# Kernel optimization log

Hardware: AMD Instinct MI355X
Metric: run time of the kernel (lower is better)

Reference implementation:

```python
import jax, jax.numpy as jnp
import numpy as np


def setup_inputs() -> dict:
    key = jax.random.key(0)
    ks = jax.random.split(key, 10)
    B, C, H, W = 2, 256, 48, 48
    Ch = 32  # C_qk // n_heads
    s = 1.0 / np.sqrt(C)
    return {
        "x": jax.random.normal(ks[0], (B, C, H, W), jnp.float32),
        "y": jax.random.normal(ks[1], (B, C, H, W), jnp.float32),
        "wq": jax.random.normal(ks[2], (C, C), jnp.float32) * s,
        "bq": jnp.zeros((C,), jnp.float32),
        "wk": jax.random.normal(ks[3], (C, C), jnp.float32) * s,
        "bk": jnp.zeros((C,), jnp.float32),
        "wv": jax.random.normal(ks[4], (C, C), jnp.float32) * s,
        "bv": jnp.zeros((C,), jnp.float32),
        "wo": jax.random.normal(ks[5], (C, C), jnp.float32) * s,
        "bo": jnp.zeros((C,), jnp.float32),
        "h_emb": jax.random.normal(ks[6], (2 * H - 1, Ch), jnp.float32),
        "w_emb": jax.random.normal(ks[7], (2 * W - 1, Ch), jnp.float32),
        "n_heads": 8,
    }


def _rel_grids(H, W):
    yi, xi = np.meshgrid(np.arange(H), np.arange(W), indexing="ij")
    rel_y = yi.reshape(1, -1) - yi.reshape(-1, 1) + (H - 1)  # [HW, HW]
    rel_x = xi.reshape(1, -1) - xi.reshape(-1, 1) + (W - 1)
    return jnp.asarray(rel_y), jnp.asarray(rel_x)


def reference(x, y, wq, bq, wk, bk, wv, bv, wo, bo, h_emb, w_emb, n_heads):
    B, C, H, W = x.shape
    HW = H * W
    C_qk = wq.shape[0]
    flat_x = x.reshape(B, C, HW)
    flat_y = y.reshape(B, C, HW)
    # 1x1 conv1d projections == matmul over channel dim
    q = jnp.einsum("oc,bcn->bon", wq, flat_x) + bq[None, :, None]
    k = jnp.einsum("oc,bcn->bon", wk, flat_y) + bk[None, :, None]
    v = jnp.einsum("oc,bcn->bon", wv, flat_y) + bv[None, :, None]
    Ch = C_qk // n_heads
    q = q.reshape(B, n_heads, Ch, HW)
    k = k.reshape(B, n_heads, Ch, HW)
    v = v.reshape(B, n_heads, Ch, HW)
    score = jnp.einsum("bhcq,bhck->bhqk", q, k)
    # relative positional bias: Q . (R_x + R_y)
    rel_y, rel_x = _rel_grids(H, W)
    r = w_emb[rel_x] + h_emb[rel_y]  # [HW, HW, Ch]
    score = score + jnp.einsum("bhci,ijc->bhij", q, r)
    score = score * (1.0 / jnp.sqrt(jnp.float32(C_qk)))
    attn = jax.nn.softmax(score, axis=-1)
    attn_out = jnp.einsum("bhqk,bhck->bhcq", attn, v).reshape(B, C, H, W)
    out = jnp.einsum("oc,bchw->bohw", wo, attn_out) + bo[None, :, None, None]
    return out
```

## Files before the change

### kernel.cpp

```cpp
#include <hip/hip_runtime.h>
#include <hip/hip_bf16.h>
#include <math.h>

#define HWN 2304
#define CC  256
#define NHD 8
#define CHD 32

#define QT_OFF 0
#define KT_OFF (2 * HWN * CC)
#define OP_OFF (2 * KT_OFF)
#define KBH_OFF (OP_OFF + 16 * HWN * CHD)
#define KBL_OFF (KBH_OFF + (16 * HWN * CHD) / 2)
#define VB_OFF  (KBL_OFF + (16 * HWN * CHD) / 2)
#define BD_OFF  (VB_OFF + 16 * HWN * CHD)

typedef __attribute__((ext_vector_type(8))) short bf16x8;
typedef __attribute__((ext_vector_type(4))) short bf16x4;
typedef __attribute__((ext_vector_type(4))) float f32x4;

__device__ inline unsigned short bf16_rne(float f) {
    unsigned int u = __float_as_uint(f);
    unsigned int r = u + 0x7FFFu + ((u >> 16) & 1u);
    return (unsigned short)(r >> 16);
}
__device__ inline float bf16_to_f(unsigned short h) {
    return __uint_as_float(((unsigned int)h) << 16);
}
__device__ inline bf16x4 bc4(int a, int b) {
    int2 t = make_int2(a, b);
    return __builtin_bit_cast(bf16x4, t);
}

__device__ inline f32x4 mfma32(bf16x8 a, bf16x8 b, f32x4 c) {
    return __builtin_amdgcn_mfma_f32_16x16x32_bf16(a, b, c, 0, 0, 0);
}
__device__ inline f32x4 mfma16(bf16x4 a, bf16x4 b, f32x4 c) {
#if __has_builtin(__builtin_amdgcn_mfma_f32_16x16x16bf16_1k)
    return __builtin_amdgcn_mfma_f32_16x16x16bf16_1k(a, b, c, 0, 0, 0);
#else
    f32x4 d;
    asm volatile("v_mfma_f32_16x16x16_bf16 %0, %1, %2, %3"
                 : "=v"(d) : "v"(a), "v"(b), "v"(c));
    return d;
#endif
}

__global__ __launch_bounds__(256) void proj_kernel(
    const float* __restrict__ x, const float* __restrict__ y,
    const float* __restrict__ wq, const float* __restrict__ bq,
    const float* __restrict__ wk, const float* __restrict__ bk,
    const float* __restrict__ wv, const float* __restrict__ bv,
    float* __restrict__ ws)
{
    const int nb = blockIdx.x * 64;
    const int ob = blockIdx.y * 64;
    const int z  = blockIdx.z;
    const int b = z / 3, which = z % 3;
    const float* in  = (which == 0) ? x : y;
    const float* W   = (which == 0) ? wq : (which == 1) ? wk : wv;
    const float* bia = (which == 0) ? bq : (which == 1) ? bk : bv;

    __shared__ float Xs[64][68];
    __shared__ float Wn[64][68];

    const int t  = threadIdx.x;
    const int tn = t & 15, to = t >> 4;
    float acc[4][4] = {};

    for (int cc = 0; cc < CC; cc += 64) {
        const int r   = t >> 4;
        const int col = (t & 15) * 4;
        #pragma unroll
        for (int rr = 0; rr < 4; rr++) {
            const int row = r + rr * 16;
            *(float4*)&Xs[row][col] =
                *(const float4*)&in[((size_t)b * CC + cc + row) * HWN + nb + col];
            *(float4*)&Wn[row][col] =
                *(const float4*)&W[(size_t)(ob + row) * CC + cc + col];
        }
        __syncthreads();
        #pragma unroll 4
        for (int k = 0; k < 64; k++) {
            float av[4];
            #pragma unroll
            for (int i2 = 0; i2 < 4; i2++) av[i2] = Wn[to * 4 + i2][k];
            const float4 b4 = *(const float4*)&Xs[k][tn * 4];
            const float bv4[4] = {b4.x, b4.y, b4.z, b4.w};
            #pragma unroll
            for (int i2 = 0; i2 < 4; i2++)
                #pragma unroll
                for (int j2 = 0; j2 < 4; j2++)
                    acc[i2][j2] = fmaf(av[i2], bv4[j2], acc[i2][j2]);
        }
        __syncthreads();
    }
    float bb[4];
    *(float4*)bb = *(const float4*)&bia[ob + to * 4];

    if (which < 2) {
        float* out = ws + ((which == 0) ? QT_OFF : KT_OFF) + (size_t)b * HWN * CC;
        #pragma unroll
        for (int j2 = 0; j2 < 4; j2++) {
            const int n = nb + tn * 4 + j2;
            float4 vo = { acc[0][j2] + bb[0], acc[1][j2] + bb[1],
                          acc[2][j2] + bb[2], acc[3][j2] + bb[3] };
            *(float4*)&out[(size_t)n * CC + ob + to * 4] = vo;
        }
    }
    if (which == 1) {
        const int o0  = ob + to * 4;
        const int b8h = b * NHD + (o0 >> 5);
        const int c0i = o0 & 31;
        unsigned short* bh_hi = (unsigned short*)(ws + KBH_OFF);
        unsigned short* bh_lo = (unsigned short*)(ws + KBL_OFF);
        #pragma unroll
        for (int j2 = 0; j2 < 4; j2++) {
            const int n = nb + tn * 4 + j2;
            unsigned int hh[2] = {0, 0}, ll[2] = {0, 0};
            #pragma unroll
            for (int i2 = 0; i2 < 4; i2++) {
                float v = acc[i2][j2] + bb[i2];
                unsigned short h = bf16_rne(v);
                unsigned short l = bf16_rne(v - bf16_to_f(h));
                hh[i2 >> 1] |= ((unsigned int)h) << ((i2 & 1) * 16);
                ll[i2 >> 1] |= ((unsigned int)l) << ((i2 & 1) * 16);
            }
            const size_t idx = ((size_t)b8h * HWN + n) * CHD + c0i;
            *(uint2*)(bh_hi + idx) = make_uint2(hh[0], hh[1]);
            *(uint2*)(bh_lo + idx) = make_uint2(ll[0], ll[1]);
        }
    } else if (which == 2) {
        const int o0  = ob + to * 4;
        const int b8h = b * NHD + (o0 >> 5);
        const int c0i = o0 & 31;
        unsigned short* vb = (unsigned short*)(ws + VB_OFF);
        #pragma unroll
        for (int i2 = 0; i2 < 4; i2++) {
            unsigned int hh[2] = {0, 0}, ll[2] = {0, 0};
            #pragma unroll
            for (int j2 = 0; j2 < 4; j2++) {
                float v = acc[i2][j2] + bb[i2];
                unsigned short h = bf16_rne(v);
                unsigned short l = bf16_rne(v - bf16_to_f(h));
                hh[j2 >> 1] |= ((unsigned int)h) << ((j2 & 1) * 16);
                ll[j2 >> 1] |= ((unsigned int)l) << ((j2 & 1) * 16);
            }
            const size_t off = (((size_t)b8h * CHD + c0i + i2) * 576
                                + (nb >> 2) + tn) * 8;
            uint4 pk = { hh[0], hh[1], ll[0], ll[1] };
            *(uint4*)(vb + off) = pk;
        }
    }
}

__global__ __launch_bounds__(256) void bounds_kernel(
    const float* __restrict__ h_emb, const float* __restrict__ w_emb,
    float* __restrict__ ws)
{
    const float* Kt = ws + KT_OFF;
    float* bounds = ws + BD_OFF;
    __shared__ float red[256];
    const int t = threadIdx.x;
    const int bh = blockIdx.x;
    if (bh < 16) {
        const int b = bh >> 3, h = bh & 7;
        float mx = 0.f;
        for (int j = t; j < HWN; j += 256) {
            const float* kp = &Kt[((size_t)b * HWN + j) * CC + h * CHD];
            float s = 0.f;
            #pragma unroll
            for (int c = 0; c < CHD; c += 4) {
                float4 v = *(const float4*)&kp[c];
                s += v.x * v.x + v.y * v.y + v.z * v.z + v.w * v.w;
            }
            mx = fmaxf(mx, s);
        }
        red[t] = mx; __syncthreads();
        for (int s2 = 128; s2 > 0; s2 >>= 1) {
            if (t < s2) red[t] = fmaxf(red[t], red[t + s2]);
            __syncthreads();
        }
        if (t == 0) bounds[bh] = sqrtf(red[0]);
    } else {
        float mw = 0.f, mh = 0.f;
        if (t < 95) {
            float s = 0.f;
            for (int c = 0; c < CHD; c++) { float v = w_emb[t * CHD + c]; s += v * v; }
            mw = s;
            s = 0.f;
            for (int c = 0; c < CHD; c++) { float v = h_emb[t * CHD + c]; s += v * v; }
            mh = s;
        }
        red[t] = mw; __syncthreads();
        for (int s2 = 128; s2 > 0; s2 >>= 1) {
            if (t < s2) red[t] = fmaxf(red[t], red[t + s2]);
            __syncthreads();
        }
        const float rw = red[0]; __syncthreads();
        red[t] = mh; __syncthreads();
        for (int s2 = 128; s2 > 0; s2 >>= 1) {
            if (t < s2) red[t] = fmaxf(red[t], red[t + s2]);
            __syncthreads();
        }
        if (t == 0) bounds[16] = sqrtf(rw) + sqrtf(red[0]);
    }
}

__global__ __launch_bounds__(256, 3) void attn_kernel(
    const float* __restrict__ h_emb, const float* __restrict__ w_emb,
    float* __restrict__ ws)
{
    const float* Qt = ws + QT_OFF;
    const float* bounds = ws + BD_OFF;
    const unsigned short* Kbh = (const unsigned short*)(ws + KBH_OFF);
    const unsigned short* Kbl = (const unsigned short*)(ws + KBL_OFF);
    const unsigned short* Vb  = (const unsigned short*)(ws + VB_OFF);
    float* OP = ws + OP_OFF;

    __shared__ float lds_a[5376];
    __shared__ float lds_b[4704];

    const int t = threadIdx.x;
    const int wv = t >> 6;
    const int lane = t & 63;
    const int il = lane & 15;
    const int g  = lane >> 4;

    const int gid = blockIdx.y * 48 + blockIdx.x;
    const int xcd = gid & 7;
    const int idx = gid >> 3;
    const int sub = idx / 48;
    const int yi  = idx - sub * 48;
    const int bh  = xcd * 2 + sub;
    const int b = bh >> 3, h = bh & 7;
    const float c1 = 0.09016844005556021f;

    bf16x8 qhi[3], qlo[3];
    float c0[3];
    {
        const float bsum = bounds[bh] + bounds[16];
        #pragma unroll
        for (int isub = 0; isub < 3; isub++) {
            const float* qp = Qt + ((size_t)(b * HWN + yi * 48 + isub * 16 + il)) * CC
                              + h * CHD + g * 8;
            float qf[8];
            *(float4*)&qf[0] = *(const float4*)qp;
            *(float4*)&qf[4] = *(const float4*)(qp + 4);
            float qn = 0.f;
            #pragma unroll
            for (int e = 0; e < 8; e++) qn = fmaf(qf[e], qf[e], qn);
            qn += __shfl_xor(qn, 16);
            qn += __shfl_xor(qn, 32);
            c0[isub] = -sqrtf(qn) * bsum * c1;
            #pragma unroll
            for (int e = 0; e < 8; e++) {
                unsigned short hh = bf16_rne(qf[e]);
                qhi[isub][e] = (short)hh;
                qlo[isub][e] = (short)bf16_rne(qf[e] - bf16_to_f(hh));
            }
        }
    }

    {
        float* tbl = (wv < 2) ? lds_a : lds_b;
        const float* emb = (wv < 2) ? w_emb : h_emb;
        const int ds0 = (wv & 1) * 3;
        #pragma unroll
        for (int dsub = ds0; dsub < ds0 + 3; dsub++) {
            int d = dsub * 16 + il;
            if (d > 94) d = 94;
            const float* ep = emb + (size_t)d * CHD + g * 8;
            float wf[8];
            *(float4*)&wf[0] = *(const float4*)ep;
            *(float4*)&wf[4] = *(const float4*)(ep + 4);
            bf16x8 whi, wlo;
            #pragma unroll
            for (int e = 0; e < 8; e++) {
                unsigned short hh = bf16_rne(wf[e]);
                whi[e] = (short)hh;
                wlo[e] = (short)bf16_rne(wf[e] - bf16_to_f(hh));
            }
            #pragma unroll
            for (int isub = 0; isub < 3; isub++) {
                f32x4 acc = {0.f, 0.f, 0.f, 0.f};
                acc = mfma32(qlo[isub], whi, acc);
                acc = mfma32(qhi[isub], wlo, acc);
                acc = mfma32(qhi[isub], whi, acc);
                #pragma unroll
                for (int r = 0; r < 4; r++)
                    tbl[(isub * 16 + 4 * g + r) * 98 + dsub * 16 + il] = c1 * acc[r];
            }
        }
    }
    __syncthreads();

    float e0[3][3][4];
    #pragma unroll
    for (int isub = 0; isub < 3; isub++) {
        const int xi = isub * 16 + il;
        #pragma unroll
        for (int jsub = 0; jsub < 3; jsub++)
            #pragma unroll
            for (int r = 0; r < 4; r++) {
                const int dx = (jsub * 16 + 4 * g + r) - xi + 47;
                e0[isub][jsub][r] = c0[isub] + lds_a[xi * 98 + dx];
            }
    }
    __syncthreads();

    f32x4 O[3][2] = {};
    float lac[3] = {0.f, 0.f, 0.f};

    #pragma unroll 1
    for (int yj = wv * 12; yj < wv * 12 + 12; ++yj) {
        const int dy = yj - yi + 47;
        float qc[3];
        #pragma unroll
        for (int isub = 0; isub < 3; isub++)
            qc[isub] = lds_b[(isub * 16 + il) * 98 + dy];

        bf16x8 khi[3], klo[3];
        #pragma unroll
        for (int jsub = 0; jsub < 3; jsub++) {
            const size_t kidx = ((size_t)bh * HWN + yj * 48 + jsub * 16 + il) * CHD + g * 8;
            khi[jsub] = *(const bf16x8*)(Kbh + kidx);
            klo[jsub] = *(const bf16x8*)(Kbl + kidx);
        }
        #pragma unroll
        for (int jsub = 0; jsub < 3; jsub++) {
            int2 ph[3], pl[3];
            #pragma unroll
            for (int isub = 0; isub < 3; isub++) {
                f32x4 acc = {0.f, 0.f, 0.f, 0.f};
                acc = mfma32(klo[jsub], qhi[isub], acc);
                acc = mfma32(khi[jsub], qlo[isub], acc);
                acc = mfma32(khi[jsub], qhi[isub], acc);
                float p[4];
                unsigned u[4];
                #pragma unroll
                for (int r = 0; r < 4; r++) {
                    const float arg = fmaf(acc[r], c1, e0[isub][jsub][r]) + qc[isub];
                    p[r] = __builtin_amdgcn_exp2f(arg);
                    u[r] = __float_as_uint(p[r]);
                }
                lac[isub] += (p[0] + p[1]) + (p[2] + p[3]);
                const unsigned h01 = __builtin_amdgcn_perm(u[1], u[0], 0x07060302u);
                const unsigned h23 = __builtin_amdgcn_perm(u[3], u[2], 0x07060302u);
                unsigned v[4];
                #pragma unroll
                for (int r = 0; r < 4; r++)
                    v[r] = __float_as_uint(p[r] - __uint_as_float(u[r] & 0xffff0000u));
                const unsigned l01 = __builtin_amdgcn_perm(v[1], v[0], 0x07060302u);
                const unsigned l23 = __builtin_amdgcn_perm(v[3], v[2], 0x07060302u);
                ph[isub] = make_int2((int)h01, (int)h23);
                pl[isub] = make_int2((int)l01, (int)l23);
            }
            #pragma unroll
            for (int csub = 0; csub < 2; csub++) {
                const size_t voff = (((size_t)bh * CHD + csub * 16 + il) * 576
                                     + yj * 12 + jsub * 4 + g) * 8;
                const int4 vv = *(const int4*)(Vb + voff);
                const bf16x4 vhi = bc4(vv.x, vv.y);
                const bf16x4 vlo = bc4(vv.z, vv.w);
                #pragma unroll
                for (int isub = 0; isub < 3; isub++) {
                    const bf16x4 pH = bc4(ph[isub].x, ph[isub].y);
                    const bf16x4 pL = bc4(pl[isub].x, pl[isub].y);
                    O[isub][csub] = mfma16(pL, vhi, O[isub][csub]);
                    O[isub][csub] = mfma16(pH, vlo, O[isub][csub]);
                    O[isub][csub] = mfma16(pH, vhi, O[isub][csub]);
                }
            }
        }
    }

    #pragma unroll
    for (int isub = 0; isub < 3; isub++) {
        lac[isub] += __shfl_xor(lac[isub], 16);
        lac[isub] += __shfl_xor(lac[isub], 32);
    }
    if (wv > 0) {
        float* cb = lds_a + ((wv - 1) * 64 + lane) * 28;
        #pragma unroll
        for (int isub = 0; isub < 3; isub++)
            #pragma unroll
            for (int csub = 0; csub < 2; csub++)
                *(f32x4*)&cb[(isub * 2 + csub) * 4] = O[isub][csub];
        cb[24] = lac[0]; cb[25] = lac[1]; cb[26] = lac[2];
    }
    __syncthreads();
    if (wv == 0) {
        #pragma unroll 1
        for (int w = 1; w < 4; w++) {
            const float* cb = lds_a + ((w - 1) * 64 + lane) * 28;
            #pragma unroll
            for (int isub = 0; isub < 3; isub++) {
                #pragma unroll
                for (int csub = 0; csub < 2; csub++)
                    O[isub][csub] += *(const f32x4*)&cb[(isub * 2 + csub) * 4];
                lac[isub] += cb[24 + isub];
            }
        }
        float inv[3][4];
        #pragma unroll
        for (int isub = 0; isub < 3; isub++)
            #pragma unroll
            for (int r = 0; r < 4; r++)
                inv[isub][r] = 1.0f / __shfl(lac[isub], 4 * g + r);
        #pragma unroll
        for (int isub = 0; isub < 3; isub++)
            #pragma unroll
            for (int csub = 0; csub < 2; csub++)
                #pragma unroll
                for (int r = 0; r < 4; r++)
                    OP[((size_t)bh * HWN + yi * 48 + isub * 16 + 4 * g + r) * CHD
                       + csub * 16 + il] = O[isub][csub][r] * inv[isub][r];
    }
}

__global__ __launch_bounds__(256) void out_kernel(
    const float* __restrict__ wo, const float* __restrict__ bo,
    const float* __restrict__ ws, float* __restrict__ out)
{
    const float* OP = ws + OP_OFF;
    const int nb = blockIdx.x * 64;
    const int ob = blockIdx.y * 64;
    const int b  = blockIdx.z;

    __shared__ float As[64][68];
    __shared__ float Wn[64][68];

    const int t = threadIdx.x;
    const int tn = t & 15, to = t >> 4;
    float acc[4][4] = {};

    for (int ci = 0; ci < 4; ci++) {
        for (int slot = t; slot < 1024; slot += 256) {
            const int n_l = slot >> 4, cq = slot & 15;
            const int h_l = ci * 2 + (cq >> 3), c_in = (cq & 7) * 4;
            const float4 u = *(const float4*)&OP[
                ((size_t)(b * NHD + h_l) * HWN + nb + n_l) * CHD + c_in];
            As[cq * 4 + 0][n_l] = u.x;
            As[cq * 4 + 1][n_l] = u.y;
            As[cq * 4 + 2][n_l] = u.z;
            As[cq * 4 + 3][n_l] = u.w;
        }
        {
            const int r = t >> 4, col = (t & 15) * 4;
            #pragma unroll
            for (int rr = 0; rr < 4; rr++) {
                const int row = r + rr * 16;
                *(float4*)&Wn[row][col] =
                    *(const float4*)&wo[(size_t)(ob + row) * CC + ci * 64 + col];
            }
        }
        __syncthreads();
        #pragma unroll 4
        for (int k = 0; k < 64; k++) {
            float av[4];
            #pragma unroll
            for (int i2 = 0; i2 < 4; i2++) av[i2] = Wn[to * 4 + i2][k];
            const float4 b4 = *(const float4*)&As[k][tn * 4];
            const float bv4[4] = {b4.x, b4.y, b4.z, b4.w};
            #pragma unroll
            for (int i2 = 0; i2 < 4; i2++)
                #pragma unroll
                for (int j2 = 0; j2 < 4; j2++)
                    acc[i2][j2] = fmaf(av[i2], bv4[j2], acc[i2][j2]);
        }
        __syncthreads();
    }
    #pragma unroll
    for (int i2 = 0; i2 < 4; i2++) {
        const int o = ob + to * 4 + i2;
        const float bb = bo[o];
        float4 vo = { acc[i2][0] + bb, acc[i2][1] + bb,
                      acc[i2][2] + bb, acc[i2][3] + bb };
        *(float4*)&out[((size_t)b * CC + o) * HWN + nb + tn * 4] = vo;
    }
}

extern "C" void kernel_launch(void* const* d_in, const int* in_sizes, int n_in,
                              void* d_out, int out_size, void* d_ws, size_t ws_size,
                              hipStream_t stream) {
    const float* x     = (const float*)d_in[0];
    const float* y     = (const float*)d_in[1];
    const float* wq    = (const float*)d_in[2];
    const float* bq    = (const float*)d_in[3];
    const float* wk    = (const float*)d_in[4];
    const float* bk    = (const float*)d_in[5];
    const float* wv    = (const float*)d_in[6];
    const float* bv    = (const float*)d_in[7];
    const float* wo    = (const float*)d_in[8];
    const float* bo    = (const float*)d_in[9];
    const float* h_emb = (const float*)d_in[10];
    const float* w_emb = (const float*)d_in[11];
    float* ws  = (float*)d_ws;
    float* out = (float*)d_out;

    dim3 gA(HWN / 64, CC / 64, 6);
    proj_kernel<<<gA, 256, 0, stream>>>(x, y, wq, bq, wk, bk, wv, bv, ws);
    bounds_kernel<<<17, 256, 0, stream>>>(h_emb, w_emb, ws);
    dim3 gC(48, 16);
    attn_kernel<<<gC, 256, 0, stream>>>(h_emb, w_emb, ws);
    dim3 gD(HWN / 64, CC / 64, 2);
    out_kernel<<<gD, 256, 0, stream>>>(wo, bo, ws, out);
}
```

Baseline: 195.5 us.

## Move projection and output GEMMs to split-bf16 MFMA with pre-converted operands

```diff
diff --git a/kernel.cpp b/kernel.cpp
--- a/kernel.cpp
+++ b/kernel.cpp
@@ -7,13 +7,20 @@
 #define NHD 8
 #define CHD 32
 
-#define QT_OFF 0
-#define KT_OFF (2 * HWN * CC)
-#define OP_OFF (2 * KT_OFF)
-#define KBH_OFF (OP_OFF + 16 * HWN * CHD)
-#define KBL_OFF (KBH_OFF + (16 * HWN * CHD) / 2)
-#define VB_OFF  (KBL_OFF + (16 * HWN * CHD) / 2)
-#define BD_OFF  (VB_OFF + 16 * HWN * CHD)
+#define SZT (2 * HWN * CC)
+#define XTH 0
+#define XTL (1 * SZT)
+#define YTH (2 * SZT)
+#define YTL (3 * SZT)
+#define QBH (4 * SZT)
+#define QBL (5 * SZT)
+#define KBH (6 * SZT)
+#define KBL (7 * SZT)
+#define VBI (8 * SZT)
+#define OBH (10 * SZT)
+#define OBL (11 * SZT)
+#define WB  (12 * SZT)
+#define BD16 (WB + 8 * 65536)
 
 typedef __attribute__((ext_vector_type(8))) short bf16x8;
 typedef __attribute__((ext_vector_type(4))) short bf16x4;
@@ -30,6 +37,12 @@
 __device__ inline bf16x4 bc4(int a, int b) {
     int2 t = make_int2(a, b);
     return __builtin_bit_cast(bf16x4, t);
+}
+__device__ inline void split2(float a, float b, unsigned& hp, unsigned& lp) {
+    unsigned short ha = bf16_rne(a), hb = bf16_rne(b);
+    hp = (unsigned)ha | ((unsigned)hb << 16);
+    lp = (unsigned)bf16_rne(a - bf16_to_f(ha))
+       | ((unsigned)bf16_rne(b - bf16_to_f(hb)) << 16);
 }
 
 __device__ inline f32x4 mfma32(bf16x8 a, bf16x8 b, f32x4 c) {
@@ -46,133 +59,165 @@
 #endif
 }
 
+__global__ __launch_bounds__(256) void prep_kernel(
+    const float* __restrict__ x, const float* __restrict__ y,
+    const float* __restrict__ wq, const float* __restrict__ wk,
+    const float* __restrict__ wv, const float* __restrict__ wo,
+    unsigned short* __restrict__ u16)
+{
+    const int t = threadIdx.x;
+    const int bid = blockIdx.x;
+    if (bid < 576) {
+        const int z = bid / 144;
+        const int r2 = bid - z * 144;
+        const int ct = r2 / 36, nt = r2 - ct * 36;
+        const int inp = z >> 1, b = z & 1;
+        const float* in = inp ? y : x;
+        unsigned short* oh = u16 + (inp ? YTH : XTH);
+        unsigned short* ol = u16 + (inp ? YTL : XTL);
+        const int nb = nt * 64, cb = ct * 64;
+        __shared__ float Xs[64][68];
+        {
+            const int row = t >> 4, col = (t & 15) * 4;
+            #pragma unroll
+            for (int rr = 0; rr < 4; rr++) {
+                const int c = row + rr * 16;
+                *(float4*)&Xs[c][col] =
+                    *(const float4*)&in[((size_t)b * CC + cb + c) * HWN + nb + col];
+            }
+        }
+        __syncthreads();
+        const int n4 = t >> 2, cg = (t & 3) * 16;
+        unsigned hh[8], ll[8];
+        #pragma unroll
+        for (int e2 = 0; e2 < 8; e2++)
+            split2(Xs[cg + 2 * e2][n4], Xs[cg + 2 * e2 + 1][n4], hh[e2], ll[e2]);
+        const size_t o0 = ((size_t)b * HWN + nb + n4) * CC + cb + cg;
+        *(uint4*)(oh + o0)     = make_uint4(hh[0], hh[1], hh[2], hh[3]);
+        *(uint4*)(oh + o0 + 8) = make_uint4(hh[4], hh[5], hh[6], hh[7]);
+        *(uint4*)(ol + o0)     = make_uint4(ll[0], ll[1], ll[2], ll[3]);
+        *(uint4*)(ol + o0 + 8) = make_uint4(ll[4], ll[5], ll[6], ll[7]);
+    } else {
+        const int bid2 = bid - 576;
+        const int w = bid2 >> 4, seg = bid2 & 15;
+        const float* W = (w == 0) ? wq : (w == 1) ? wk : (w == 2) ? wv : wo;
+        unsigned short* wh = u16 + WB + w * 131072;
+        unsigned short* wl = wh + 65536;
+        const int i0 = seg * 4096 + t * 16;
+        float v[16];
+        #pragma unroll
+        for (int j = 0; j < 4; j++)
+            *(float4*)&v[j * 4] = *(const float4*)&W[i0 + j * 4];
+        unsigned hh[8], ll[8];
+        #pragma unroll
+        for (int e2 = 0; e2 < 8; e2++)
+            split2(v[2 * e2], v[2 * e2 + 1], hh[e2], ll[e2]);
+        *(uint4*)(wh + i0)     = make_uint4(hh[0], hh[1], hh[2], hh[3]);
+        *(uint4*)(wh + i0 + 8) = make_uint4(hh[4], hh[5], hh[6], hh[7]);
+        *(uint4*)(wl + i0)     = make_uint4(ll[0], ll[1], ll[2], ll[3]);
+        *(uint4*)(wl + i0 + 8) = make_uint4(ll[4], ll[5], ll[6], ll[7]);
+    }
+}
+
 __global__ __launch_bounds__(256) void proj_kernel(
-    const float* __restrict__ x, const float* __restrict__ y,
-    const float* __restrict__ wq, const float* __restrict__ bq,
-    const float* __restrict__ wk, const float* __restrict__ bk,
-    const float* __restrict__ wv, const float* __restrict__ bv,
-    float* __restrict__ ws)
+    const float* __restrict__ bq, const float* __restrict__ bk,
+    const float* __restrict__ bv, unsigned short* __restrict__ u16)
 {
-    const int nb = blockIdx.x * 64;
-    const int ob = blockIdx.y * 64;
-    const int z  = blockIdx.z;
-    const int b = z / 3, which = z % 3;
-    const float* in  = (which == 0) ? x : y;
-    const float* W   = (which == 0) ? wq : (which == 1) ? wk : wv;
-    const float* bia = (which == 0) ? bq : (which == 1) ? bk : bv;
-
-    __shared__ float Xs[64][68];
-    __shared__ float Wn[64][68];
-
-    const int t  = threadIdx.x;
-    const int tn = t & 15, to = t >> 4;
-    float acc[4][4] = {};
-
-    for (int cc = 0; cc < CC; cc += 64) {
-        const int r   = t >> 4;
-        const int col = (t & 15) * 4;
-        #pragma unroll
-        for (int rr = 0; rr < 4; rr++) {
-            const int row = r + rr * 16;
-            *(float4*)&Xs[row][col] =
-                *(const float4*)&in[((size_t)b * CC + cc + row) * HWN + nb + col];
-            *(float4*)&Wn[row][col] =
-                *(const float4*)&W[(size_t)(ob + row) * CC + cc + col];
-        }
-        __syncthreads();
-        #pragma unroll 4
-        for (int k = 0; k < 64; k++) {
-            float av[4];
-            #pragma unroll
-            for (int i2 = 0; i2 < 4; i2++) av[i2] = Wn[to * 4 + i2][k];
-            const float4 b4 = *(const float4*)&Xs[k][tn * 4];
-            const float bv4[4] = {b4.x, b4.y, b4.z, b4.w};
-            #pragma unroll
-            for (int i2 = 0; i2 < 4; i2++)
-                #pragma unroll
-                for (int j2 = 0; j2 < 4; j2++)
-                    acc[i2][j2] = fmaf(av[i2], bv4[j2], acc[i2][j2]);
-        }
-        __syncthreads();
-    }
-    float bb[4];
-    *(float4*)bb = *(const float4*)&bia[ob + to * 4];
-
-    if (which < 2) {
-        float* out = ws + ((which == 0) ? QT_OFF : KT_OFF) + (size_t)b * HWN * CC;
-        #pragma unroll
-        for (int j2 = 0; j2 < 4; j2++) {
-            const int n = nb + tn * 4 + j2;
-            float4 vo = { acc[0][j2] + bb[0], acc[1][j2] + bb[1],
-                          acc[2][j2] + bb[2], acc[3][j2] + bb[3] };
-            *(float4*)&out[(size_t)n * CC + ob + to * 4] = vo;
-        }
-    }
-    if (which == 1) {
-        const int o0  = ob + to * 4;
-        const int b8h = b * NHD + (o0 >> 5);
-        const int c0i = o0 & 31;
-        unsigned short* bh_hi = (unsigned short*)(ws + KBH_OFF);
-        unsigned short* bh_lo = (unsigned short*)(ws + KBL_OFF);
-        #pragma unroll
-        for (int j2 = 0; j2 < 4; j2++) {
-            const int n = nb + tn * 4 + j2;
-            unsigned int hh[2] = {0, 0}, ll[2] = {0, 0};
-            #pragma unroll
-            for (int i2 = 0; i2 < 4; i2++) {
-                float v = acc[i2][j2] + bb[i2];
-                unsigned short h = bf16_rne(v);
-                unsigned short l = bf16_rne(v - bf16_to_f(h));
-                hh[i2 >> 1] |= ((unsigned int)h) << ((i2 & 1) * 16);
-                ll[i2 >> 1] |= ((unsigned int)l) << ((i2 & 1) * 16);
-            }
-            const size_t idx = ((size_t)b8h * HWN + n) * CHD + c0i;
-            *(uint2*)(bh_hi + idx) = make_uint2(hh[0], hh[1]);
-            *(uint2*)(bh_lo + idx) = make_uint2(ll[0], ll[1]);
-        }
-    } else if (which == 2) {
-        const int o0  = ob + to * 4;
-        const int b8h = b * NHD + (o0 >> 5);
-        const int c0i = o0 & 31;
-        unsigned short* vb = (unsigned short*)(ws + VB_OFF);
-        #pragma unroll
-        for (int i2 = 0; i2 < 4; i2++) {
-            unsigned int hh[2] = {0, 0}, ll[2] = {0, 0};
-            #pragma unroll
-            for (int j2 = 0; j2 < 4; j2++) {
-                float v = acc[i2][j2] + bb[i2];
-                unsigned short h = bf16_rne(v);
-                unsigned short l = bf16_rne(v - bf16_to_f(h));
-                hh[j2 >> 1] |= ((unsigned int)h) << ((j2 & 1) * 16);
-                ll[j2 >> 1] |= ((unsigned int)l) << ((j2 & 1) * 16);
-            }
-            const size_t off = (((size_t)b8h * CHD + c0i + i2) * 576
-                                + (nb >> 2) + tn) * 8;
-            uint4 pk = { hh[0], hh[1], ll[0], ll[1] };
-            *(uint4*)(vb + off) = pk;
+    const int nt = blockIdx.x, ot = blockIdx.y, z = blockIdx.z;
+    const int b = z / 3, which = z - b * 3;
+    const unsigned short* Xh = u16 + (which == 0 ? XTH : YTH);
+    const unsigned short* Xl = u16 + (which == 0 ? XTL : YTL);
+    const unsigned short* Wh = u16 + WB + which * 131072;
+    const unsigned short* Wl = Wh + 65536;
+    const float* bias = (which == 0) ? bq : (which == 1) ? bk : bv;
+    const int t = threadIdx.x, w4 = t >> 6, lane = t & 63;
+    const int il = lane & 15, g = lane >> 4;
+    const int nb = nt * 64, ob = ot * 64 + w4 * 16;
+
+    f32x4 acc[4] = {};
+    const size_t xbase = ((size_t)b * HWN + nb + il) * CC;
+    const size_t wbase = (size_t)(ob + il) * CC;
+    for (int kc = 0; kc < 256; kc += 32) {
+        const size_t wi = wbase + kc + g * 8;
+        const bf16x8 whi = *(const bf16x8*)(Wh + wi);
+        const bf16x8 wlo = *(const bf16x8*)(Wl + wi);
+        #pragma unroll
+        for (int ns = 0; ns < 4; ns++) {
+            const size_t xi = xbase + (size_t)ns * 16 * CC + kc + g * 8;
+            const bf16x8 xhi = *(const bf16x8*)(Xh + xi);
+            const bf16x8 xlo = *(const bf16x8*)(Xl + xi);
+            if (which != 2)
+                acc[ns] = mfma32(whi, xhi, mfma32(whi, xlo, mfma32(wlo, xhi, acc[ns])));
+            else
+                acc[ns] = mfma32(xhi, whi, mfma32(xlo, whi, mfma32(xhi, wlo, acc[ns])));
+        }
+    }
+    const int bh = b * NHD + ot * 2 + (w4 >> 1);
+    if (which != 2) {
+        const int c0 = (w4 & 1) * 16 + 4 * g;
+        float bb4[4];
+        *(float4*)bb4 = *(const float4*)&bias[ob + 4 * g];
+        unsigned short* Oh = u16 + (which == 0 ? QBH : KBH);
+        unsigned short* Ol = u16 + (which == 0 ? QBL : KBL);
+        #pragma unroll
+        for (int ns = 0; ns < 4; ns++) {
+            const int n = nb + ns * 16 + il;
+            unsigned hh[2], ll[2];
+            #pragma unroll
+            for (int r = 0; r < 2; r++)
+                split2(acc[ns][2 * r] + bb4[2 * r], acc[ns][2 * r + 1] + bb4[2 * r + 1],
+                       hh[r], ll[r]);
+            const size_t oi = ((size_t)bh * HWN + n) * CHD + c0;
+            *(uint2*)(Oh + oi) = make_uint2(hh[0], hh[1]);
+            *(uint2*)(Ol + oi) = make_uint2(ll[0], ll[1]);
+        }
+    } else {
+        const int c = (w4 & 1) * 16 + il;
+        const float bb = bias[ot * 64 + w4 * 16 + il];
+        unsigned short* vb = u16 + VBI;
+        #pragma unroll
+        for (int ns = 0; ns < 4; ns++) {
+            const int jg = nb / 4 + ns * 4 + g;
+            unsigned hh[2], ll[2];
+            #pragma unroll
+            for (int r = 0; r < 2; r++)
+                split2(acc[ns][2 * r] + bb, acc[ns][2 * r + 1] + bb, hh[r], ll[r]);
+            *(uint4*)(vb + (((size_t)bh * CHD + c) * 576 + jg) * 8) =
+                make_uint4(hh[0], hh[1], ll[0], ll[1]);
         }
     }
 }
 
 __global__ __launch_bounds__(256) void bounds_kernel(
     const float* __restrict__ h_emb, const float* __restrict__ w_emb,
-    float* __restrict__ ws)
+    unsigned short* __restrict__ u16)
 {
-    const float* Kt = ws + KT_OFF;
-    float* bounds = ws + BD_OFF;
+    float* bounds = (float*)(u16 + BD16);
     __shared__ float red[256];
     const int t = threadIdx.x;
     const int bh = blockIdx.x;
     if (bh < 16) {
-        const int b = bh >> 3, h = bh & 7;
+        const unsigned short* kh = u16 + KBH;
+        const unsigned short* kl = u16 + KBL;
         float mx = 0.f;
         for (int j = t; j < HWN; j += 256) {
-            const float* kp = &Kt[((size_t)b * HWN + j) * CC + h * CHD];
+            const size_t base = ((size_t)bh * HWN + j) * CHD;
             float s = 0.f;
             #pragma unroll
-            for (int c = 0; c < CHD; c += 4) {
-                float4 v = *(const float4*)&kp[c];
-                s += v.x * v.x + v.y * v.y + v.z * v.z + v.w * v.w;
+            for (int q2 = 0; q2 < 4; q2++) {
+                const uint4 H = *(const uint4*)(kh + base + q2 * 8);
+                const uint4 L = *(const uint4*)(kl + base + q2 * 8);
+                const unsigned hw[4] = {H.x, H.y, H.z, H.w};
+                const unsigned lw[4] = {L.x, L.y, L.z, L.w};
+                #pragma unroll
+                for (int m = 0; m < 4; m++) {
+                    const float v0 = bf16_to_f((unsigned short)(hw[m] & 0xffffu))
+                                   + bf16_to_f((unsigned short)(lw[m] & 0xffffu));
+                    const float v1 = bf16_to_f((unsigned short)(hw[m] >> 16))
+                                   + bf16_to_f((unsigned short)(lw[m] >> 16));
+                    s = fmaf(v0, v0, s);
+                    s = fmaf(v1, v1, s);
+                }
             }
             mx = fmaxf(mx, s);
         }
@@ -209,14 +254,12 @@
 
 __global__ __launch_bounds__(256, 3) void attn_kernel(
     const float* __restrict__ h_emb, const float* __restrict__ w_emb,
-    float* __restrict__ ws)
+    unsigned short* __restrict__ u16)
 {
-    const float* Qt = ws + QT_OFF;
-    const float* bounds = ws + BD_OFF;
-    const unsigned short* Kbh = (const unsigned short*)(ws + KBH_OFF);
-    const unsigned short* Kbl = (const unsigned short*)(ws + KBL_OFF);
-    const unsigned short* Vb  = (const unsigned short*)(ws + VB_OFF);
-    float* OP = ws + OP_OFF;
+    const float* bounds = (const float*)(u16 + BD16);
+    const unsigned short* Kbh = u16 + KBH;
+    const unsigned short* Kbl = u16 + KBL;
+    const unsigned short* Vb  = u16 + VBI;
 
     __shared__ float lds_a[5376];
     __shared__ float lds_b[4704];
@@ -233,32 +276,29 @@
     const int sub = idx / 48;
     const int yi  = idx - sub * 48;
     const int bh  = xcd * 2 + sub;
-    const int b = bh >> 3, h = bh & 7;
     const float c1 = 0.09016844005556021f;
 
     bf16x8 qhi[3], qlo[3];
     float c0[3];
     {
+        const unsigned short* Qh = u16 + QBH;
+        const unsigned short* Ql = u16 + QBL;
         const float bsum = bounds[bh] + bounds[16];
         #pragma unroll
         for (int isub = 0; isub < 3; isub++) {
-            const float* qp = Qt + ((size_t)(b * HWN + yi * 48 + isub * 16 + il)) * CC
-                              + h * CHD + g * 8;
-            float qf[8];
-            *(float4*)&qf[0] = *(const float4*)qp;
-            *(float4*)&qf[4] = *(const float4*)(qp + 4);
+            const size_t qi = ((size_t)bh * HWN + yi * 48 + isub * 16 + il) * CHD + g * 8;
+            qhi[isub] = *(const bf16x8*)(Qh + qi);
+            qlo[isub] = *(const bf16x8*)(Ql + qi);
             float qn = 0.f;
             #pragma unroll
-            for (int e = 0; e < 8; e++) qn = fmaf(qf[e], qf[e], qn);
+            for (int e = 0; e < 8; e++) {
+                const float v = bf16_to_f((unsigned short)qhi[isub][e])
+                              + bf16_to_f((unsigned short)qlo[isub][e]);
+                qn = fmaf(v, v, qn);
+            }
             qn += __shfl_xor(qn, 16);
             qn += __shfl_xor(qn, 32);
             c0[isub] = -sqrtf(qn) * bsum * c1;
-            #pragma unroll
-            for (int e = 0; e < 8; e++) {
-                unsigned short hh = bf16_rne(qf[e]);
-                qhi[isub][e] = (short)hh;
-                qlo[isub][e] = (short)bf16_rne(qf[e] - bf16_to_f(hh));
-            }
         }
     }
 
@@ -277,9 +317,9 @@
             bf16x8 whi, wlo;
             #pragma unroll
             for (int e = 0; e < 8; e++) {
-                unsigned short hh = bf16_rne(wf[e]);
-                whi[e] = (short)hh;
-                wlo[e] = (short)bf16_rne(wf[e] - bf16_to_f(hh));
+                unsigned short hhw = bf16_rne(wf[e]);
+                whi[e] = (short)hhw;
+                wlo[e] = (short)bf16_rne(wf[e] - bf16_to_f(hhw));
             }
             #pragma unroll
             for (int isub = 0; isub < 3; isub++) {
@@ -383,11 +423,12 @@
     if (wv > 0) {
         float* cb = lds_a + ((wv - 1) * 64 + lane) * 28;
         #pragma unroll
-        for (int isub = 0; isub < 3; isub++)
+        for (int isub = 0; isub < 3; isub++) {
             #pragma unroll
             for (int csub = 0; csub < 2; csub++)
                 *(f32x4*)&cb[(isub * 2 + csub) * 4] = O[isub][csub];
-        cb[24] = lac[0]; cb[25] = lac[1]; cb[26] = lac[2];
+            cb[24 + isub] = lac[isub];
+        }
     }
     __syncthreads();
     if (wv == 0) {
@@ -408,77 +449,59 @@
             #pragma unroll
             for (int r = 0; r < 4; r++)
                 inv[isub][r] = 1.0f / __shfl(lac[isub], 4 * g + r);
+        unsigned short* Obh = u16 + OBH;
+        unsigned short* Obl = u16 + OBL;
         #pragma unroll
         for (int isub = 0; isub < 3; isub++)
             #pragma unroll
             for (int csub = 0; csub < 2; csub++)
                 #pragma unroll
-                for (int r = 0; r < 4; r++)
-                    OP[((size_t)bh * HWN + yi * 48 + isub * 16 + 4 * g + r) * CHD
-                       + csub * 16 + il] = O[isub][csub][r] * inv[isub][r];
+                for (int r = 0; r < 4; r++) {
+                    const float v = O[isub][csub][r] * inv[isub][r];
+                    const unsigned short hv = bf16_rne(v);
+                    const size_t oi =
+                        ((size_t)bh * HWN + yi * 48 + isub * 16 + 4 * g + r) * CHD
+                        + csub * 16 + il;
+                    Obh[oi] = hv;
+                    Obl[oi] = bf16_rne(v - bf16_to_f(hv));
+                }
     }
 }
 
 __global__ __launch_bounds__(256) void out_kernel(
-    const float* __restrict__ wo, const float* __restrict__ bo,
-    const float* __restrict__ ws, float* __restrict__ out)
+    const float* __restrict__ bo, const unsigned short* __restrict__ u16,
+    float* __restrict__ out)
 {
-    const float* OP = ws + OP_OFF;
-    const int nb = blockIdx.x * 64;
-    const int ob = blockIdx.y * 64;
-    const int b  = blockIdx.z;
-
-    __shared__ float As[64][68];
-    __shared__ float Wn[64][68];
-
-    const int t = threadIdx.x;
-    const int tn = t & 15, to = t >> 4;
-    float acc[4][4] = {};
-
-    for (int ci = 0; ci < 4; ci++) {
-        for (int slot = t; slot < 1024; slot += 256) {
-            const int n_l = slot >> 4, cq = slot & 15;
-            const int h_l = ci * 2 + (cq >> 3), c_in = (cq & 7) * 4;
-            const float4 u = *(const float4*)&OP[
-                ((size_t)(b * NHD + h_l) * HWN + nb + n_l) * CHD + c_in];
-            As[cq * 4 + 0][n_l] = u.x;
-            As[cq * 4 + 1][n_l] = u.y;
-            As[cq * 4 + 2][n_l] = u.z;
-            As[cq * 4 + 3][n_l] = u.w;
-        }
-        {
-            const int r = t >> 4, col = (t & 15) * 4;
-            #pragma unroll
-            for (int rr = 0; rr < 4; rr++) {
-                const int row = r + rr * 16;
-                *(float4*)&Wn[row][col] =
-                    *(const float4*)&wo[(size_t)(ob + row) * CC + ci * 64 + col];
-            }
-        }
-        __syncthreads();
-        #pragma unroll 4
-        for (int k = 0; k < 64; k++) {
-            float av[4];
-            #pragma unroll
-            for (int i2 = 0; i2 < 4; i2++) av[i2] = Wn[to * 4 + i2][k];
-            const float4 b4 = *(const float4*)&As[k][tn * 4];
-            const float bv4[4] = {b4.x, b4.y, b4.z, b4.w};
-            #pragma unroll
-            for (int i2 = 0; i2 < 4; i2++)
-                #pragma unroll
-                for (int j2 = 0; j2 < 4; j2++)
-                    acc[i2][j2] = fmaf(av[i2], bv4[j2], acc[i2][j2]);
-        }
-        __syncthreads();
-    }
+    const int nt = blockIdx.x, ot = blockIdx.y, b = blockIdx.z;
+    const int t = threadIdx.x, w4 = t >> 6, lane = t & 63;
+    const int il = lane & 15, g = lane >> 4;
+    const int nb = nt * 32, ob = ot * 64 + w4 * 16;
+    const unsigned short* Oh = u16 + OBH;
+    const unsigned short* Ol = u16 + OBL;
+    const unsigned short* Wh = u16 + WB + 3 * 131072;
+    const unsigned short* Wl = Wh + 65536;
+    f32x4 acc[2] = {};
     #pragma unroll
-    for (int i2 = 0; i2 < 4; i2++) {
-        const int o = ob + to * 4 + i2;
-        const float bb = bo[o];
-        float4 vo = { acc[i2][0] + bb, acc[i2][1] + bb,
-                      acc[i2][2] + bb, acc[i2][3] + bb };
-        *(float4*)&out[((size_t)b * CC + o) * HWN + nb + tn * 4] = vo;
-    }
+    for (int h = 0; h < 8; h++) {
+        const size_t wi = (size_t)(ob + il) * CC + h * 32 + g * 8;
+        const bf16x8 whi = *(const bf16x8*)(Wh + wi);
+        const bf16x8 wlo = *(const bf16x8*)(Wl + wi);
+        #pragma unroll
+        for (int ns = 0; ns < 2; ns++) {
+            const size_t xi = ((size_t)(b * NHD + h) * HWN + nb + ns * 16 + il) * CHD + g * 8;
+            const bf16x8 xhi = *(const bf16x8*)(Oh + xi);
+            const bf16x8 xlo = *(const bf16x8*)(Ol + xi);
+            acc[ns] = mfma32(whi, xhi, mfma32(whi, xlo, mfma32(wlo, xhi, acc[ns])));
+        }
+    }
+    float bb4[4];
+    *(float4*)bb4 = *(const float4*)&bo[ob + 4 * g];
+    #pragma unroll
+    for (int ns = 0; ns < 2; ns++)
+        #pragma unroll
+        for (int r = 0; r < 4; r++)
+            out[((size_t)(b * CC + ob + 4 * g + r)) * HWN + nb + ns * 16 + il]
+                = acc[ns][r] + bb4[r];
 }
 
 extern "C" void kernel_launch(void* const* d_in, const int* in_sizes, int n_in,
@@ -490,20 +513,18 @@
     const float* bq    = (const float*)d_in[3];
     const float* wk    = (const float*)d_in[4];
     const float* bk    = (const float*)d_in[5];
-    const float* wv    = (const float*)d_in[6];
+    const float* wvp   = (const float*)d_in[6];
     const float* bv    = (const float*)d_in[7];
     const float* wo    = (const float*)d_in[8];
     const float* bo    = (const float*)d_in[9];
     const float* h_emb = (const float*)d_in[10];
     const float* w_emb = (const float*)d_in[11];
-    float* ws  = (float*)d_ws;
+    unsigned short* u16 = (unsigned short*)d_ws;
     float* out = (float*)d_out;
 
-    dim3 gA(HWN / 64, CC / 64, 6);
-    proj_kernel<<<gA, 256, 0, stream>>>(x, y, wq, bq, wk, bk, wv, bv, ws);
-    bounds_kernel<<<17, 256, 0, stream>>>(h_emb, w_emb, ws);
-    dim3 gC(48, 16);
-    attn_kernel<<<gC, 256, 0, stream>>>(h_emb, w_emb, ws);
-    dim3 gD(HWN / 64, CC / 64, 2);
-    out_kernel<<<gD, 256, 0, stream>>>(wo, bo, ws, out);
-}
+    prep_kernel<<<640, 256, 0, stream>>>(x, y, wq, wk, wvp, wo, u16);
+    proj_kernel<<<dim3(36, 4, 6), 256, 0, stream>>>(bq, bk, bv, u16);
+    bounds_kernel<<<17, 256, 0, stream>>>(h_emb, w_emb, u16);
+    attn_kernel<<<dim3(48, 16), 256, 0, stream>>>(h_emb, w_emb, u16);
+    out_kernel<<<dim3(72, 4, 2), 256, 0, stream>>>(bo, u16, out);
+}
```

After: 194.5 us. Within noise of the previous version (-0.5%).
